# Kernel optimization log

Measured on AMD Instinct MI355X. Metric: run time of the kernel, lower is better.

## Reference

```python
import jax, jax.numpy as jnp
import numpy as np

FP8_E4M3_MAX = 448.0  # max_value for fp8 e4m3fn in the torch module


def _to_fp8_e4m3(x):
    # round-to-nearest fp8 e4m3fn values, represented back in fp32
    return x.astype(jnp.float8_e4m3fn).astype(jnp.float32)


def setup_inputs() -> dict:
    key = jax.random.key(0)
    k1, k2, k3 = jax.random.split(key, 3)
    B, S, K, N = 4, 2048, 4096, 14336
    x = jax.random.normal(k1, (B, S, K), dtype=jnp.float32)
    # per-tensor scales (QParamsLinear enforces per_tensor qscheme for this path)
    weight_scale = jnp.array([0.01], dtype=jnp.float32)
    input_scale = jnp.array([0.02], dtype=jnp.float32)
    # weight stored in real-quantized fp8 form (values are exact e4m3 lattice points)
    w_fp = jax.random.normal(k2, (N, K), dtype=jnp.float32)
    weight_q = _to_fp8_e4m3(jnp.clip(w_fp / weight_scale, -FP8_E4M3_MAX, FP8_E4M3_MAX))
    bias = jax.random.normal(k3, (N,), dtype=jnp.float32)
    return {"x": x, "weight_q": weight_q, "weight_scale": weight_scale,
            "input_scale": input_scale, "bias": bias}


def reference(x, weight_q, weight_scale, input_scale, bias):
    # Quantize activation: divide by per-tensor scale, clamp to fp8 range, cast to e4m3
    qx = jnp.clip(x / input_scale, -FP8_E4M3_MAX, FP8_E4M3_MAX)
    qx = qx.astype(jnp.float8_e4m3fn).astype(x.dtype)
    # scaled_mm: (qx @ weight_q.T) * (input_scale * weight_scale) + bias
    out = jnp.einsum("bsk,nk->bsn", qx, weight_q.astype(x.dtype))
    out = out * (input_scale * weight_scale)[0] + bias
    return out
```

## Files before the change

kernel.cpp:

```cpp
#include <hip/hip_runtime.h>
#include <stdint.h>

typedef float f32x4  __attribute__((ext_vector_type(4)));
typedef float f32x16 __attribute__((ext_vector_type(16)));
typedef int   i32x4  __attribute__((ext_vector_type(4)));
typedef int   i32x8  __attribute__((ext_vector_type(8)));

constexpr int Mdim = 8192;
constexpr int Ndim = 14336;
constexpr int Kdim = 4096;
constexpr int BM = 256, BN = 256, BK = 128;
constexpr int NT = Kdim / BK;
constexpr uint32_t BUFSZ = 65536;

#define VMCNT(n) asm volatile("s_waitcnt vmcnt(" #n ")" ::: "memory")
#define LGKM0()  do { asm volatile("s_waitcnt lgkmcnt(0)" ::: "memory"); \
                      __builtin_amdgcn_sched_barrier(0); } while (0)
#define BARRIER() do { asm volatile("" ::: "memory"); \
                       __builtin_amdgcn_s_barrier(); \
                       asm volatile("" ::: "memory"); } while (0)

__device__ __forceinline__ void gload_lds16(const void* g, void* l) {
  __builtin_amdgcn_global_load_lds(
      (const __attribute__((address_space(1))) unsigned int*)g,
      (__attribute__((address_space(3))) unsigned int*)l, 16, 0, 0);
}

__device__ __forceinline__ i32x4 ldsr128(const uint8_t* p) {
  i32x4 r;
  asm volatile("ds_read_b128 %0, %1"
               : "=v"(r)
               : "v"((const __attribute__((address_space(3))) uint8_t*)p));
  return r;
}

__device__ __forceinline__ i32x8 frag(const uint8_t* tile, int row, int kb) {
  const int p0 = kb ^ ((row & 7) << 4);
  const uint8_t* rp = tile + row * BK;
  i32x4 lo = ldsr128(rp + p0);
  i32x4 hi = ldsr128(rp + (p0 ^ 16));
  return __builtin_shufflevector(lo, hi, 0, 1, 2, 3, 4, 5, 6, 7);
}

__device__ __forceinline__ f32x16 mx(i32x8 a, i32x8 b, f32x16 c) {
  return __builtin_amdgcn_mfma_scale_f32_32x32x64_f8f6f4(
      a, b, c, 0, 0, 0, 0x7f7f7f7f, 0, 0x7f7f7f7f);
}

__global__ void __launch_bounds__(256) quant_fp8_kernel(
    const float* __restrict__ in, uint8_t* __restrict__ out8,
    const float* __restrict__ scale_ptr, long long n)
{
  const float s = scale_ptr ? scale_ptr[0] : 1.0f;
  const long long nch = n >> 3;
  const long long idx = (long long)blockIdx.x * blockDim.x + threadIdx.x;
  const long long stride = (long long)gridDim.x * blockDim.x;
  for (long long c = idx; c < nch; c += stride) {
    f32x4 v0 = *(const f32x4*)(in + c * 8);
    f32x4 v1 = *(const f32x4*)(in + c * 8 + 4);
    float q[8];
#pragma unroll
    for (int j = 0; j < 4; ++j) {
      q[j]     = fminf(fmaxf(v0[j] / s, -448.f), 448.f);
      q[4 + j] = fminf(fmaxf(v1[j] / s, -448.f), 448.f);
    }
    unsigned int w0 = 0, w1 = 0;
    w0 = __builtin_amdgcn_cvt_pk_fp8_f32(q[0], q[1], w0, false);
    w0 = __builtin_amdgcn_cvt_pk_fp8_f32(q[2], q[3], w0, true);
    w1 = __builtin_amdgcn_cvt_pk_fp8_f32(q[4], q[5], w1, false);
    w1 = __builtin_amdgcn_cvt_pk_fp8_f32(q[6], q[7], w1, true);
    uint2 r; r.x = w0; r.y = w1;
    *(uint2*)(out8 + c * 8) = r;
  }
}

__global__ void __launch_bounds__(512, 2) gemm_fp8_kernel(
    const uint8_t* __restrict__ qa, const uint8_t* __restrict__ qb,
    const float* __restrict__ iscale, const float* __restrict__ wscale,
    const float* __restrict__ bias, float* __restrict__ out)
{
  __shared__ uint8_t smem[2 * BUFSZ];

  const int tid  = threadIdx.x;
  const int wave = tid >> 6;
  const int lane = tid & 63;
  const int wm   = wave >> 2;
  const int wn   = wave & 3;
  const int col  = lane & 31;
  const int kh   = lane >> 5;
  const long long tile_m = (long long)blockIdx.y * BM;
  const long long tile_n = (long long)blockIdx.x * BN;

  const int urow = tid >> 3;
  const int pbs  = tid & 7;
  const int scol = (pbs ^ (urow & 7)) << 4;
  const uint8_t* gA = qa + (tile_m + urow) * Kdim + scol;
  const uint8_t* gB = qb + (tile_n + urow) * Kdim + scol;
  uint8_t* lbase = smem + wave * 1024;

#define STAGE(u, mat, k0, boff)                                           \
  gload_lds16((mat ? gB : gA) + (long long)(u) * 64 * Kdim + (k0),        \
              lbase + (boff) + (mat) * 32768 + (u) * 8192)

  f32x16 acc[4][2] = {};

  const int rowA = wm * 128 + col;
  const int rowB = wn * 64 + col;
  const int kb0 = kh * 32;
  const int kb1 = 64 + kh * 32;

#pragma unroll
  for (int u = 0; u < 4; ++u) STAGE(u, 0, 0, 0);
#pragma unroll
  for (int u = 0; u < 4; ++u) STAGE(u, 1, 0, 0);

  uint32_t cur = 0;
  for (int t = 0; t < NT - 1; ++t) {
    const long long kn = (long long)(t + 1) * BK;
    const uint32_t nxt = cur ^ BUFSZ;
    const uint8_t* Ab = smem + cur;
    const uint8_t* Bb = smem + cur + 32768;

    STAGE(0, 0, kn, nxt); STAGE(1, 0, kn, nxt);
    VMCNT(2);
    BARRIER();
    i32x8 a0 = frag(Ab, rowA +  0, kb0);
    i32x8 a1 = frag(Ab, rowA + 32, kb0);
    i32x8 b0 = frag(Bb, rowB +  0, kb0);
    i32x8 b1 = frag(Bb, rowB + 32, kb0);
    LGKM0();
    __builtin_amdgcn_s_setprio(1);
    acc[0][0] = mx(a0, b0, acc[0][0]);  acc[0][1] = mx(a0, b1, acc[0][1]);
    acc[1][0] = mx(a1, b0, acc[1][0]);  acc[1][1] = mx(a1, b1, acc[1][1]);
    __builtin_amdgcn_s_setprio(0);

    STAGE(2, 0, kn, nxt); STAGE(3, 0, kn, nxt);
    a0 = frag(Ab, rowA + 64, kb0);
    a1 = frag(Ab, rowA + 96, kb0);
    LGKM0();
    __builtin_amdgcn_s_setprio(1);
    acc[2][0] = mx(a0, b0, acc[2][0]);  acc[2][1] = mx(a0, b1, acc[2][1]);
    acc[3][0] = mx(a1, b0, acc[3][0]);  acc[3][1] = mx(a1, b1, acc[3][1]);
    __builtin_amdgcn_s_setprio(0);

    STAGE(0, 1, kn, nxt); STAGE(1, 1, kn, nxt);
    a0 = frag(Ab, rowA +  0, kb1);
    a1 = frag(Ab, rowA + 32, kb1);
    b0 = frag(Bb, rowB +  0, kb1);
    b1 = frag(Bb, rowB + 32, kb1);
    LGKM0();
    __builtin_amdgcn_s_setprio(1);
    acc[0][0] = mx(a0, b0, acc[0][0]);  acc[0][1] = mx(a0, b1, acc[0][1]);
    acc[1][0] = mx(a1, b0, acc[1][0]);  acc[1][1] = mx(a1, b1, acc[1][1]);
    __builtin_amdgcn_s_setprio(0);

    STAGE(2, 1, kn, nxt); STAGE(3, 1, kn, nxt);
    a0 = frag(Ab, rowA + 64, kb1);
    a1 = frag(Ab, rowA + 96, kb1);
    LGKM0();
    __builtin_amdgcn_s_setprio(1);
    acc[2][0] = mx(a0, b0, acc[2][0]);  acc[2][1] = mx(a0, b1, acc[2][1]);
    acc[3][0] = mx(a1, b0, acc[3][0]);  acc[3][1] = mx(a1, b1, acc[3][1]);
    __builtin_amdgcn_s_setprio(0);
    BARRIER();

    cur = nxt;
  }

  {
    const uint8_t* Ab = smem + cur;
    const uint8_t* Bb = smem + cur + 32768;
    VMCNT(0);
    BARRIER();
#pragma unroll
    for (int ks = 0; ks < 2; ++ks) {
      const int kb = ks * 64 + kh * 32;
      i32x8 b0 = frag(Bb, rowB +  0, kb);
      i32x8 b1 = frag(Bb, rowB + 32, kb);
#pragma unroll
      for (int m = 0; m < 4; ++m) {
        i32x8 a = frag(Ab, rowA + m * 32, kb);
        LGKM0();
        acc[m][0] = mx(a, b0, acc[m][0]);
        acc[m][1] = mx(a, b1, acc[m][1]);
      }
    }
  }

  const float alpha = iscale[0] * wscale[0];
  const long long col0 = tile_n + wn * 64 + col;
  const float bv0 = bias[col0];
  const float bv1 = bias[col0 + 32];
#pragma unroll
  for (int m = 0; m < 4; ++m) {
#pragma unroll
    for (int r = 0; r < 16; ++r) {
      const long long row =
          tile_m + wm * 128 + m * 32 + (r & 3) + 8 * (r >> 2) + 4 * kh;
      float* op = out + row * (long long)Ndim + col0;
      op[0]  = acc[m][0][r] * alpha + bv0;
      op[32] = acc[m][1][r] * alpha + bv1;
    }
  }
#undef STAGE
}

extern "C" void kernel_launch(void* const* d_in, const int* in_sizes, int n_in,
                              void* d_out, int out_size, void* d_ws, size_t ws_size,
                              hipStream_t stream) {
  const float* x      = (const float*)d_in[0];
  const float* weight = (const float*)d_in[1];
  const float* wscale = (const float*)d_in[2];
  const float* iscale = (const float*)d_in[3];
  const float* bias   = (const float*)d_in[4];
  float* out = (float*)d_out;

  uint8_t* qx = (uint8_t*)d_ws;
  uint8_t* qw = qx + (long long)Mdim * Kdim;

  const long long nx = (long long)Mdim * Kdim;
  const long long nw = (long long)Ndim * Kdim;

  quant_fp8_kernel<<<4096, 256, 0, stream>>>(x, qx, iscale, nx);
  quant_fp8_kernel<<<4096, 256, 0, stream>>>(weight, qw, nullptr, nw);

  dim3 grid(Ndim / BN, Mdim / BM);
  gemm_fp8_kernel<<<grid, 512, 0, stream>>>(qx, qw, iscale, wscale, bias, out);
}
```

Baseline: 522.8 us.

## Software-pipeline LDS fragment reads with partial lgkmcnt waits and XCD-aware block swizzle

Restructures the inner K loop so LDS fragment reads for the next MFMA group are issued before the current group's MFMAs. It waits with partial lgkmcnt counts instead of draining to zero, so LDS latency overlaps with matrix math. It also flattens the grid to 1D and remaps block IDs so consecutive tiles land on the same XCD (bid&7 chunking), aiming for better L2 reuse. The cost is more live fragment registers, which puts pressure on the 2-blocks-per-CU occupancy target.

```diff
diff --git a/kernel.cpp b/kernel.cpp
--- a/kernel.cpp
+++ b/kernel.cpp
@@ -11,10 +11,12 @@
 constexpr int Kdim = 4096;
 constexpr int BM = 256, BN = 256, BK = 128;
 constexpr int NT = Kdim / BK;
+constexpr int NTN = Ndim / BN;
+constexpr int NTM = Mdim / BM;
 constexpr uint32_t BUFSZ = 65536;
 
 #define VMCNT(n) asm volatile("s_waitcnt vmcnt(" #n ")" ::: "memory")
-#define LGKM0()  do { asm volatile("s_waitcnt lgkmcnt(0)" ::: "memory"); \
+#define LGKM(n)  do { asm volatile("s_waitcnt lgkmcnt(" #n ")" ::: "memory"); \
                       __builtin_amdgcn_sched_barrier(0); } while (0)
 #define BARRIER() do { asm volatile("" ::: "memory"); \
                        __builtin_amdgcn_s_barrier(); \
@@ -81,6 +83,11 @@
 {
   __shared__ uint8_t smem[2 * BUFSZ];
 
+  const int bid = blockIdx.x;
+  const int swz = (bid & 7) * (NTM * NTN / 8) + (bid >> 3);
+  const int mt  = swz / NTN;
+  const int ntl = swz - mt * NTN;
+
   const int tid  = threadIdx.x;
   const int wave = tid >> 6;
   const int lane = tid & 63;
@@ -88,8 +95,8 @@
   const int wn   = wave & 3;
   const int col  = lane & 31;
   const int kh   = lane >> 5;
-  const long long tile_m = (long long)blockIdx.y * BM;
-  const long long tile_n = (long long)blockIdx.x * BN;
+  const long long tile_m = (long long)mt * BM;
+  const long long tile_n = (long long)ntl * BN;
 
   const int urow = tid >> 3;
   const int pbs  = tid & 7;
@@ -124,43 +131,43 @@
     STAGE(0, 0, kn, nxt); STAGE(1, 0, kn, nxt);
     VMCNT(2);
     BARRIER();
-    i32x8 a0 = frag(Ab, rowA +  0, kb0);
-    i32x8 a1 = frag(Ab, rowA + 32, kb0);
-    i32x8 b0 = frag(Bb, rowB +  0, kb0);
-    i32x8 b1 = frag(Bb, rowB + 32, kb0);
-    LGKM0();
-    __builtin_amdgcn_s_setprio(1);
-    acc[0][0] = mx(a0, b0, acc[0][0]);  acc[0][1] = mx(a0, b1, acc[0][1]);
-    acc[1][0] = mx(a1, b0, acc[1][0]);  acc[1][1] = mx(a1, b1, acc[1][1]);
-    __builtin_amdgcn_s_setprio(0);
-
+
+    i32x8 A0 = frag(Ab, rowA +  0, kb0);
+    i32x8 A1 = frag(Ab, rowA + 32, kb0);
+    i32x8 B0 = frag(Bb, rowB +  0, kb0);
+    i32x8 B1 = frag(Bb, rowB + 32, kb0);
     STAGE(2, 0, kn, nxt); STAGE(3, 0, kn, nxt);
-    a0 = frag(Ab, rowA + 64, kb0);
-    a1 = frag(Ab, rowA + 96, kb0);
-    LGKM0();
-    __builtin_amdgcn_s_setprio(1);
-    acc[2][0] = mx(a0, b0, acc[2][0]);  acc[2][1] = mx(a0, b1, acc[2][1]);
-    acc[3][0] = mx(a1, b0, acc[3][0]);  acc[3][1] = mx(a1, b1, acc[3][1]);
+    i32x8 A2 = frag(Ab, rowA + 64, kb0);
+    i32x8 A3 = frag(Ab, rowA + 96, kb0);
+    LGKM(4);
+    __builtin_amdgcn_s_setprio(1);
+    acc[0][0] = mx(A0, B0, acc[0][0]);  acc[0][1] = mx(A0, B1, acc[0][1]);
+    acc[1][0] = mx(A1, B0, acc[1][0]);  acc[1][1] = mx(A1, B1, acc[1][1]);
     __builtin_amdgcn_s_setprio(0);
 
     STAGE(0, 1, kn, nxt); STAGE(1, 1, kn, nxt);
-    a0 = frag(Ab, rowA +  0, kb1);
-    a1 = frag(Ab, rowA + 32, kb1);
-    b0 = frag(Bb, rowB +  0, kb1);
-    b1 = frag(Bb, rowB + 32, kb1);
-    LGKM0();
-    __builtin_amdgcn_s_setprio(1);
-    acc[0][0] = mx(a0, b0, acc[0][0]);  acc[0][1] = mx(a0, b1, acc[0][1]);
-    acc[1][0] = mx(a1, b0, acc[1][0]);  acc[1][1] = mx(a1, b1, acc[1][1]);
+    i32x8 A0p = frag(Ab, rowA +  0, kb1);
+    i32x8 A1p = frag(Ab, rowA + 32, kb1);
+    i32x8 B0p = frag(Bb, rowB +  0, kb1);
+    i32x8 B1p = frag(Bb, rowB + 32, kb1);
+    LGKM(8);
+    __builtin_amdgcn_s_setprio(1);
+    acc[2][0] = mx(A2, B0, acc[2][0]);  acc[2][1] = mx(A2, B1, acc[2][1]);
+    acc[3][0] = mx(A3, B0, acc[3][0]);  acc[3][1] = mx(A3, B1, acc[3][1]);
     __builtin_amdgcn_s_setprio(0);
 
     STAGE(2, 1, kn, nxt); STAGE(3, 1, kn, nxt);
-    a0 = frag(Ab, rowA + 64, kb1);
-    a1 = frag(Ab, rowA + 96, kb1);
-    LGKM0();
-    __builtin_amdgcn_s_setprio(1);
-    acc[2][0] = mx(a0, b0, acc[2][0]);  acc[2][1] = mx(a0, b1, acc[2][1]);
-    acc[3][0] = mx(a1, b0, acc[3][0]);  acc[3][1] = mx(a1, b1, acc[3][1]);
+    i32x8 A2p = frag(Ab, rowA + 64, kb1);
+    i32x8 A3p = frag(Ab, rowA + 96, kb1);
+    LGKM(4);
+    __builtin_amdgcn_s_setprio(1);
+    acc[0][0] = mx(A0p, B0p, acc[0][0]);  acc[0][1] = mx(A0p, B1p, acc[0][1]);
+    acc[1][0] = mx(A1p, B0p, acc[1][0]);  acc[1][1] = mx(A1p, B1p, acc[1][1]);
+    __builtin_amdgcn_s_setprio(0);
+    LGKM(0);
+    __builtin_amdgcn_s_setprio(1);
+    acc[2][0] = mx(A2p, B0p, acc[2][0]);  acc[2][1] = mx(A2p, B1p, acc[2][1]);
+    acc[3][0] = mx(A3p, B0p, acc[3][0]);  acc[3][1] = mx(A3p, B1p, acc[3][1]);
     __builtin_amdgcn_s_setprio(0);
     BARRIER();
 
@@ -172,19 +179,30 @@
     const uint8_t* Bb = smem + cur + 32768;
     VMCNT(0);
     BARRIER();
-#pragma unroll
-    for (int ks = 0; ks < 2; ++ks) {
-      const int kb = ks * 64 + kh * 32;
-      i32x8 b0 = frag(Bb, rowB +  0, kb);
-      i32x8 b1 = frag(Bb, rowB + 32, kb);
-#pragma unroll
-      for (int m = 0; m < 4; ++m) {
-        i32x8 a = frag(Ab, rowA + m * 32, kb);
-        LGKM0();
-        acc[m][0] = mx(a, b0, acc[m][0]);
-        acc[m][1] = mx(a, b1, acc[m][1]);
-      }
-    }
+    i32x8 A0 = frag(Ab, rowA +  0, kb0);
+    i32x8 A1 = frag(Ab, rowA + 32, kb0);
+    i32x8 B0 = frag(Bb, rowB +  0, kb0);
+    i32x8 B1 = frag(Bb, rowB + 32, kb0);
+    i32x8 A2 = frag(Ab, rowA + 64, kb0);
+    i32x8 A3 = frag(Ab, rowA + 96, kb0);
+    LGKM(4);
+    acc[0][0] = mx(A0, B0, acc[0][0]);  acc[0][1] = mx(A0, B1, acc[0][1]);
+    acc[1][0] = mx(A1, B0, acc[1][0]);  acc[1][1] = mx(A1, B1, acc[1][1]);
+    i32x8 A0p = frag(Ab, rowA +  0, kb1);
+    i32x8 A1p = frag(Ab, rowA + 32, kb1);
+    i32x8 B0p = frag(Bb, rowB +  0, kb1);
+    i32x8 B1p = frag(Bb, rowB + 32, kb1);
+    LGKM(8);
+    acc[2][0] = mx(A2, B0, acc[2][0]);  acc[2][1] = mx(A2, B1, acc[2][1]);
+    acc[3][0] = mx(A3, B0, acc[3][0]);  acc[3][1] = mx(A3, B1, acc[3][1]);
+    i32x8 A2p = frag(Ab, rowA + 64, kb1);
+    i32x8 A3p = frag(Ab, rowA + 96, kb1);
+    LGKM(4);
+    acc[0][0] = mx(A0p, B0p, acc[0][0]);  acc[0][1] = mx(A0p, B1p, acc[0][1]);
+    acc[1][0] = mx(A1p, B0p, acc[1][0]);  acc[1][1] = mx(A1p, B1p, acc[1][1]);
+    LGKM(0);
+    acc[2][0] = mx(A2p, B0p, acc[2][0]);  acc[2][1] = mx(A2p, B1p, acc[2][1]);
+    acc[3][0] = mx(A3p, B0p, acc[3][0]);  acc[3][1] = mx(A3p, B1p, acc[3][1]);
   }
 
   const float alpha = iscale[0] * wscale[0];
@@ -224,6 +242,5 @@
   quant_fp8_kernel<<<4096, 256, 0, stream>>>(x, qx, iscale, nx);
   quant_fp8_kernel<<<4096, 256, 0, stream>>>(weight, qw, nullptr, nw);
 
-  dim3 grid(Ndim / BN, Mdim / BM);
-  gemm_fp8_kernel<<<grid, 512, 0, stream>>>(qx, qw, iscale, wscale, bias, out);
-}
+  gemm_fp8_kernel<<<NTM * NTN, 512, 0, stream>>>(qx, qw, iscale, wscale, bias, out);
+}
```

Result: slower. 552.3 us (+5.6%).

## Switch GEMM to BK=64 with four-slot, three-deep prefetch pipeline

Applied to the files above, without the earlier changes.

Halves the K tile to 64 and replaces the double-buffered loop with a four-slot ring buffer that keeps three tiles in flight, issuing all loads for tile t+3 right after the barrier. A new swizzle matched to the 64-byte rows reduces LDS bank conflicts. A partial lgkmcnt wait lets the first MFMAs start before all fragments arrive. The aim is to hide global-load latency better, at the cost of twice as many barriers per K and the same 128KB of LDS.

```diff
diff --git a/kernel.cpp b/kernel.cpp
--- a/kernel.cpp
+++ b/kernel.cpp
@@ -9,12 +9,12 @@
 constexpr int Mdim = 8192;
 constexpr int Ndim = 14336;
 constexpr int Kdim = 4096;
-constexpr int BM = 256, BN = 256, BK = 128;
+constexpr int BM = 256, BN = 256, BK = 64;
 constexpr int NT = Kdim / BK;
-constexpr uint32_t BUFSZ = 65536;
+constexpr uint32_t SLOT = 32768;
 
 #define VMCNT(n) asm volatile("s_waitcnt vmcnt(" #n ")" ::: "memory")
-#define LGKM0()  do { asm volatile("s_waitcnt lgkmcnt(0)" ::: "memory"); \
+#define LGKM(n)  do { asm volatile("s_waitcnt lgkmcnt(" #n ")" ::: "memory"); \
                       __builtin_amdgcn_sched_barrier(0); } while (0)
 #define BARRIER() do { asm volatile("" ::: "memory"); \
                        __builtin_amdgcn_s_barrier(); \
@@ -34,9 +34,9 @@
   return r;
 }
 
-__device__ __forceinline__ i32x8 frag(const uint8_t* tile, int row, int kb) {
-  const int p0 = kb ^ ((row & 7) << 4);
-  const uint8_t* rp = tile + row * BK;
+__device__ __forceinline__ i32x8 frag(const uint8_t* tile, int row, int kh) {
+  const int p0 = (kh * 32) ^ (((row >> 1) & 3) << 4);
+  const uint8_t* rp = tile + row * 64;
   i32x4 lo = ldsr128(rp + p0);
   i32x4 hi = ldsr128(rp + (p0 ^ 16));
   return __builtin_shufflevector(lo, hi, 0, 1, 2, 3, 4, 5, 6, 7);
@@ -79,7 +79,7 @@
     const float* __restrict__ iscale, const float* __restrict__ wscale,
     const float* __restrict__ bias, float* __restrict__ out)
 {
-  __shared__ uint8_t smem[2 * BUFSZ];
+  __shared__ uint8_t smem[4 * SLOT];
 
   const int tid  = threadIdx.x;
   const int wave = tid >> 6;
@@ -91,100 +91,61 @@
   const long long tile_m = (long long)blockIdx.y * BM;
   const long long tile_n = (long long)blockIdx.x * BN;
 
-  const int urow = tid >> 3;
-  const int pbs  = tid & 7;
-  const int scol = (pbs ^ (urow & 7)) << 4;
+  const int urow = tid >> 2;
+  const int pbs  = tid & 3;
+  const int scol = (pbs ^ ((urow >> 1) & 3)) << 4;
   const uint8_t* gA = qa + (tile_m + urow) * Kdim + scol;
   const uint8_t* gB = qb + (tile_n + urow) * Kdim + scol;
   uint8_t* lbase = smem + wave * 1024;
 
-#define STAGE(u, mat, k0, boff)                                           \
-  gload_lds16((mat ? gB : gA) + (long long)(u) * 64 * Kdim + (k0),        \
-              lbase + (boff) + (mat) * 32768 + (u) * 8192)
+#define STAGE(u, mat, tt, boff)                                            \
+  gload_lds16((mat ? gB : gA) + (long long)(u) * 128 * Kdim +              \
+                  (long long)(tt) * BK,                                    \
+              lbase + (boff) + (mat) * 16384 + (u) * 8192)
 
   f32x16 acc[4][2] = {};
 
   const int rowA = wm * 128 + col;
   const int rowB = wn * 64 + col;
-  const int kb0 = kh * 32;
-  const int kb1 = 64 + kh * 32;
 
 #pragma unroll
-  for (int u = 0; u < 4; ++u) STAGE(u, 0, 0, 0);
-#pragma unroll
-  for (int u = 0; u < 4; ++u) STAGE(u, 1, 0, 0);
+  for (int tt = 0; tt < 3; ++tt) {
+    STAGE(0, 0, tt, (uint32_t)tt * SLOT); STAGE(1, 0, tt, (uint32_t)tt * SLOT);
+    STAGE(0, 1, tt, (uint32_t)tt * SLOT); STAGE(1, 1, tt, (uint32_t)tt * SLOT);
+  }
 
-  uint32_t cur = 0;
-  for (int t = 0; t < NT - 1; ++t) {
-    const long long kn = (long long)(t + 1) * BK;
-    const uint32_t nxt = cur ^ BUFSZ;
-    const uint8_t* Ab = smem + cur;
-    const uint8_t* Bb = smem + cur + 32768;
+  for (int t = 0; t < NT; ++t) {
+    const uint8_t* Ab = smem + (uint32_t)(t & 3) * SLOT;
+    const uint8_t* Bb = Ab + 16384;
 
-    STAGE(0, 0, kn, nxt); STAGE(1, 0, kn, nxt);
-    VMCNT(2);
-    BARRIER();
-    i32x8 a0 = frag(Ab, rowA +  0, kb0);
-    i32x8 a1 = frag(Ab, rowA + 32, kb0);
-    i32x8 b0 = frag(Bb, rowB +  0, kb0);
-    i32x8 b1 = frag(Bb, rowB + 32, kb0);
-    LGKM0();
-    __builtin_amdgcn_s_setprio(1);
-    acc[0][0] = mx(a0, b0, acc[0][0]);  acc[0][1] = mx(a0, b1, acc[0][1]);
-    acc[1][0] = mx(a1, b0, acc[1][0]);  acc[1][1] = mx(a1, b1, acc[1][1]);
-    __builtin_amdgcn_s_setprio(0);
-
-    STAGE(2, 0, kn, nxt); STAGE(3, 0, kn, nxt);
-    a0 = frag(Ab, rowA + 64, kb0);
-    a1 = frag(Ab, rowA + 96, kb0);
-    LGKM0();
-    __builtin_amdgcn_s_setprio(1);
-    acc[2][0] = mx(a0, b0, acc[2][0]);  acc[2][1] = mx(a0, b1, acc[2][1]);
-    acc[3][0] = mx(a1, b0, acc[3][0]);  acc[3][1] = mx(a1, b1, acc[3][1]);
-    __builtin_amdgcn_s_setprio(0);
-
-    STAGE(0, 1, kn, nxt); STAGE(1, 1, kn, nxt);
-    a0 = frag(Ab, rowA +  0, kb1);
-    a1 = frag(Ab, rowA + 32, kb1);
-    b0 = frag(Bb, rowB +  0, kb1);
-    b1 = frag(Bb, rowB + 32, kb1);
-    LGKM0();
-    __builtin_amdgcn_s_setprio(1);
-    acc[0][0] = mx(a0, b0, acc[0][0]);  acc[0][1] = mx(a0, b1, acc[0][1]);
-    acc[1][0] = mx(a1, b0, acc[1][0]);  acc[1][1] = mx(a1, b1, acc[1][1]);
-    __builtin_amdgcn_s_setprio(0);
-
-    STAGE(2, 1, kn, nxt); STAGE(3, 1, kn, nxt);
-    a0 = frag(Ab, rowA + 64, kb1);
-    a1 = frag(Ab, rowA + 96, kb1);
-    LGKM0();
-    __builtin_amdgcn_s_setprio(1);
-    acc[2][0] = mx(a0, b0, acc[2][0]);  acc[2][1] = mx(a0, b1, acc[2][1]);
-    acc[3][0] = mx(a1, b0, acc[3][0]);  acc[3][1] = mx(a1, b1, acc[3][1]);
-    __builtin_amdgcn_s_setprio(0);
+    if (t + 2 < NT)      { VMCNT(8); }
+    else if (t + 1 < NT) { VMCNT(4); }
+    else                 { VMCNT(0); }
     BARRIER();
 
-    cur = nxt;
-  }
+    if (t + 3 < NT) {
+      const uint32_t bo = (uint32_t)((t + 3) & 3) * SLOT;
+      STAGE(0, 0, t + 3, bo); STAGE(1, 0, t + 3, bo);
+      STAGE(0, 1, t + 3, bo); STAGE(1, 1, t + 3, bo);
+    }
 
-  {
-    const uint8_t* Ab = smem + cur;
-    const uint8_t* Bb = smem + cur + 32768;
-    VMCNT(0);
-    BARRIER();
-#pragma unroll
-    for (int ks = 0; ks < 2; ++ks) {
-      const int kb = ks * 64 + kh * 32;
-      i32x8 b0 = frag(Bb, rowB +  0, kb);
-      i32x8 b1 = frag(Bb, rowB + 32, kb);
-#pragma unroll
-      for (int m = 0; m < 4; ++m) {
-        i32x8 a = frag(Ab, rowA + m * 32, kb);
-        LGKM0();
-        acc[m][0] = mx(a, b0, acc[m][0]);
-        acc[m][1] = mx(a, b1, acc[m][1]);
-      }
-    }
+    i32x8 A0 = frag(Ab, rowA +  0, kh);
+    i32x8 A1 = frag(Ab, rowA + 32, kh);
+    i32x8 B0 = frag(Bb, rowB +  0, kh);
+    i32x8 B1 = frag(Bb, rowB + 32, kh);
+    i32x8 A2 = frag(Ab, rowA + 64, kh);
+    i32x8 A3 = frag(Ab, rowA + 96, kh);
+
+    LGKM(4);
+    __builtin_amdgcn_s_setprio(1);
+    acc[0][0] = mx(A0, B0, acc[0][0]);  acc[0][1] = mx(A0, B1, acc[0][1]);
+    acc[1][0] = mx(A1, B0, acc[1][0]);  acc[1][1] = mx(A1, B1, acc[1][1]);
+    __builtin_amdgcn_s_setprio(0);
+    LGKM(0);
+    __builtin_amdgcn_s_setprio(1);
+    acc[2][0] = mx(A2, B0, acc[2][0]);  acc[2][1] = mx(A2, B1, acc[2][1]);
+    acc[3][0] = mx(A3, B0, acc[3][0]);  acc[3][1] = mx(A3, B1, acc[3][1]);
+    __builtin_amdgcn_s_setprio(0);
   }
 
   const float alpha = iscale[0] * wscale[0];
```

Result: slower. 570.2 us (+9.1%).
